# Kernel optimization log

Hardware: AMD Instinct MI355X
Metric: run time of the kernel (lower is better)

Reference implementation:

```python
import jax, jax.numpy as jnp
import numpy as np

N_NODES = 50000
EPS = 1e-12  # F.normalize eps


def _gcn_layer(x, W, b, src, dst):
    # GCNConv(normalize=False): h = x @ W, then sum-aggregate messages from
    # source nodes into target nodes along edge_index, then add bias.
    h = x @ W
    agg = jax.ops.segment_sum(h[src], dst, num_segments=N_NODES)
    out = agg + b
    # F.normalize(p=2, dim=-1) then ReLU
    norm = jnp.linalg.norm(out, axis=-1, keepdims=True)
    out = out / jnp.maximum(norm, EPS)
    return jax.nn.relu(out)


def setup_inputs() -> dict:
    key = jax.random.key(0)
    ks = jax.random.split(key, 8)
    nfeat, nhid, nclass, n_edges = 128, 128, 40, 640000
    x = jax.random.normal(ks[0], (N_NODES, nfeat), dtype=jnp.float32)
    edge_index = jax.random.randint(ks[1], (2, n_edges), 0, N_NODES, dtype=jnp.int64)
    s = 1.0 / np.sqrt(nhid)
    return {
        "x": x,
        "edge_index": edge_index,
        "W1": jax.random.normal(ks[2], (nfeat, nhid), jnp.float32) * s,
        "b1": jnp.zeros((nhid,), jnp.float32),
        "W2": jax.random.normal(ks[3], (nhid, nhid), jnp.float32) * s,
        "b2": jnp.zeros((nhid,), jnp.float32),
        "W3": jax.random.normal(ks[4], (nhid, nhid), jnp.float32) * s,
        "b3": jnp.zeros((nhid,), jnp.float32),
        "W4": jax.random.normal(ks[5], (nhid, nhid), jnp.float32) * s,
        "b4": jnp.zeros((nhid,), jnp.float32),
        "Wl": jax.random.normal(ks[6], (nhid, nclass), jnp.float32) * s,
        "bl": jnp.zeros((nclass,), jnp.float32),
    }


def reference(x, edge_index, W1, b1, W2, b2, W3, b3, W4, b4, Wl, bl):
    src, dst = edge_index[0], edge_index[1]
    x1 = _gcn_layer(x, W1, b1, src, dst)
    x2 = _gcn_layer(x1, W2, b2, src, dst)
    x3 = _gcn_layer(x2, W3, b3, src, dst)
    x4 = _gcn_layer(x3, W4, b4, src, dst)
    logits = x4 @ Wl + bl
    probs = jax.nn.softmax(logits, axis=-1)
    return (logits, probs, x4)
```

## Files before the change

kernel.cpp:

```cpp
#include <hip/hip_runtime.h>
#include <hip/hip_bf16.h>
#include <hip/hip_fp16.h>
#include <math.h>

#define NFEAT 128
#define NCLASS 40
#define RSHIFT 12
#define NRANGE 13

typedef __attribute__((ext_vector_type(8))) short frag_ab;
typedef __attribute__((ext_vector_type(4))) float frag_cd;

static __device__ inline unsigned short f2bf_rne(float f) {
    union { float f; unsigned u; } v;
    v.f = f;
    unsigned r = v.u + 0x7FFFu + ((v.u >> 16) & 1u);
    return (unsigned short)(r >> 16);
}
static __device__ inline float bf2f(unsigned short h) {
    union { unsigned u; float f; } v;
    v.u = ((unsigned)h) << 16;
    return v.f;
}


__global__ __launch_bounds__(256) void prep_kernel(const float* __restrict__ x,
                                                   __half* __restrict__ xh, int xc4,
                                                   const float* __restrict__ W0,
                                                   const float* __restrict__ W1,
                                                   const float* __restrict__ W2,
                                                   const float* __restrict__ W3,
                                                   short* __restrict__ whi,
                                                   short* __restrict__ wlo,
                                                   const int* __restrict__ src,
                                                   const int* __restrict__ dst,
                                                   int* __restrict__ cntR, int n_nodes,
                                                   int n_edges, int convB) {
    int b = blockIdx.x;
    if (b < convB) {
        int i = b * 256 + threadIdx.x;
        if (i < xc4) {
            float4 v = ((const float4*)x)[i];
            ((__half2*)xh)[i * 2 + 0] = __floats2half2_rn(v.x, v.y);
            ((__half2*)xh)[i * 2 + 1] = __floats2half2_rn(v.z, v.w);
        }
    } else if (b < convB + 32) {
        int wb = b - convB;
        int layer = wb >> 3;
        const float* W = layer == 0 ? W0 : layer == 1 ? W1 : layer == 2 ? W2 : W3;
        short* h = whi + (size_t)layer * 16384;
        short* l = wlo + (size_t)layer * 16384;
        int idx = (wb & 7) * 256 + threadIdx.x;
        int lane = idx & 63;
        int t = (idx >> 6) & 7;
        int s = idx >> 9;
        int quad = lane >> 4;
        int n = lane & 15;
        int kbase = s * 32 + quad * 8;
        int col = t * 16 + n;
#pragma unroll
        for (int j = 0; j < 8; ++j) {
            float f = W[(size_t)(kbase + j) * NFEAT + col];
            unsigned short hb = f2bf_rne(f);
            unsigned short lb = f2bf_rne(f - bf2f(hb));
            h[(size_t)idx * 8 + j] = (short)hb;
            l[(size_t)idx * 8 + j] = (short)lb;
        }
    } else {
        int hb = b - convB - 32;
        int i = hb * 256 + threadIdx.x;
        int n4 = n_edges >> 2;
        if (i < n4) {
            int4 d = ((const int4*)dst)[i];
            int4 s = ((const int4*)src)[i];
            atomicAdd(&cntR[(size_t)(s.x >> RSHIFT) * n_nodes + d.x], 1);
            atomicAdd(&cntR[(size_t)(s.y >> RSHIFT) * n_nodes + d.y], 1);
            atomicAdd(&cntR[(size_t)(s.z >> RSHIFT) * n_nodes + d.z], 1);
            atomicAdd(&cntR[(size_t)(s.w >> RSHIFT) * n_nodes + d.w], 1);
        }
        if (hb == 0 && threadIdx.x == 0) {
            for (int e = n4 << 2; e < n_edges; ++e)
                atomicAdd(&cntR[(size_t)(src[e] >> RSHIFT) * n_nodes + dst[e]], 1);
        }
    }
}


__global__ __launch_bounds__(256) void scan1_kernel(const int* __restrict__ cntR,
                                                    int* __restrict__ cnt,
                                                    int* __restrict__ excl,
                                                    int* __restrict__ bsums,
                                                    int* __restrict__ hist, int n) {
    __shared__ int sd[256];
    __shared__ int lh[64];
    int t = threadIdx.x;
    int i = blockIdx.x * 256 + t;
    if (t < 64) lh[t] = 0;
    int v = 0;
    if (i < n) {
#pragma unroll
        for (int r = 0; r < NRANGE; ++r) v += cntR[(size_t)r * n + i];
    }
    sd[t] = v;
    __syncthreads();
#pragma unroll
    for (int off = 1; off < 256; off <<= 1) {
        int tmp = (t >= off) ? sd[t - off] : 0;
        __syncthreads();
        sd[t] += tmp;
        __syncthreads();
    }
    if (i < n) {
        cnt[i] = v;
        excl[i] = sd[t] - v;
        atomicAdd(&lh[v < 63 ? v : 63], 1);
    }
    if (t == 255) bsums[blockIdx.x] = sd[255];
    __syncthreads();
    if (t < 64 && lh[t]) atomicAdd(&hist[t], lh[t]);
}

__global__ __launch_bounds__(256) void scan3_kernel(const int* __restrict__ excl,
                                                    const int* __restrict__ bsums,
                                                    int* __restrict__ row_ptr,
                                                    const int* __restrict__ cntR,
                                                    int* __restrict__ woffR,
                                                    const int* __restrict__ cnt,
                                                    const int* __restrict__ hist,
                                                    int* __restrict__ hoff,
                                                    int* __restrict__ perm,
                                                    int n, int nb) {
    __shared__ int sd[256];
    __shared__ int off_s, tot_s;
    __shared__ int hincl[64];
    __shared__ int bcnt[64];
    __shared__ int bbase[64];
    int t = threadIdx.x;
    if (t < 64) bcnt[t] = 0;
    int v = (t < nb) ? bsums[t] : 0;
    sd[t] = v;
    __syncthreads();
#pragma unroll
    for (int off = 1; off < 256; off <<= 1) {
        int tmp = (t >= off) ? sd[t - off] : 0;
        __syncthreads();
        sd[t] += tmp;
        __syncthreads();
    }
    if (t == 0) {
        off_s = (blockIdx.x > 0) ? sd[blockIdx.x - 1] : 0;
        tot_s = sd[255];
        int s = 0;
        for (int d = 0; d < 64; ++d) { s += hist[d]; hincl[d] = s; }
    }
    __syncthreads();
    int i = blockIdx.x * 256 + t;
    int d = 0, myslot = 0;
    if (i < n) {
        int val = excl[i] + off_s;
        row_ptr[i] = val;
        int run = val;
#pragma unroll
        for (int r = 0; r < NRANGE; ++r) {
            int c = cntR[(size_t)r * n + i];
            woffR[(size_t)r * n + i] = run;
            run += c;
        }
        int deg = cnt[i];
        d = deg < 63 ? deg : 63;
        myslot = atomicAdd(&bcnt[d], 1);
    }
    if (i == 0) row_ptr[n] = tot_s;
    __syncthreads();
    if (t < 64 && bcnt[t]) bbase[t] = atomicAdd(&hoff[t], bcnt[t]);
    __syncthreads();
    if (i < n) {
        perm[(n - hincl[d]) + bbase[d] + myslot] = i;
    }
}

__global__ __launch_bounds__(256) void scatter_kernel(const int* __restrict__ src,
                                                      const int* __restrict__ dst,
                                                      int* __restrict__ woffR,
                                                      int* __restrict__ src_sorted,
                                                      int n_nodes, int n_edges) {
    int i = blockIdx.x * 256 + threadIdx.x;
    int n4 = n_edges >> 2;
    if (i < n4) {
        int4 d = ((const int4*)dst)[i];
        int4 s = ((const int4*)src)[i];
        int p0 = atomicAdd(&woffR[(size_t)(s.x >> RSHIFT) * n_nodes + d.x], 1);
        int p1 = atomicAdd(&woffR[(size_t)(s.y >> RSHIFT) * n_nodes + d.y], 1);
        int p2 = atomicAdd(&woffR[(size_t)(s.z >> RSHIFT) * n_nodes + d.z], 1);
        int p3 = atomicAdd(&woffR[(size_t)(s.w >> RSHIFT) * n_nodes + d.w], 1);
        src_sorted[p0] = s.x;
        src_sorted[p1] = s.y;
        src_sorted[p2] = s.z;
        src_sorted[p3] = s.w;
    }
    if (i == 0) {
        for (int e = n4 << 2; e < n_edges; ++e) {
            int p = atomicAdd(&woffR[(size_t)(src[e] >> RSHIFT) * n_nodes + dst[e]], 1);
            src_sorted[p] = src[e];
        }
    }
}


__global__ __launch_bounds__(256) void gcn_fused_kernel(const __half* __restrict__ xin,
                                                        const int* __restrict__ row_ptr,
                                                        const int* __restrict__ src_sorted,
                                                        const int* __restrict__ perm,
                                                        const short* __restrict__ whi,
                                                        const short* __restrict__ wlo,
                                                        const float* __restrict__ bias,
                                                        float* __restrict__ outf,
                                                        __half* __restrict__ outh, int M) {
    __shared__ float smem[64][132];
    __shared__ int ctr;
    int tid = threadIdx.x;
    int base = blockIdx.x * 64;
    if (tid == 0) ctr = 0;
    __syncthreads();

    {
        int c = tid & 15;
        int lane = tid & 63;
        const uint4* xp = (const uint4*)xin;
        for (;;) {
            int nl = 0;
            if ((lane & 15) == 0) nl = atomicAdd(&ctr, 1);
            nl = __shfl(nl, lane & 48);
            if (nl >= 64) break;
            int slot = base + nl;
            float a[8];
#pragma unroll
            for (int i = 0; i < 8; ++i) a[i] = 0.f;
            int jb = 0, je = 0;
            if (slot < M) {
                int node = perm[slot];
                jb = row_ptr[node];
                je = row_ptr[node + 1];
            }

            int j = jb;
            int i0 = 0, i1 = 0, i2 = 0, i3 = 0;
            bool have4 = (j + 4 <= je);
            if (have4) {
                i0 = src_sorted[j];
                i1 = src_sorted[j + 1];
                i2 = src_sorted[j + 2];
                i3 = src_sorted[j + 3];
            }
            while (have4) {
                uint4 r0 = xp[i0 * 16 + c];
                uint4 r1 = xp[i1 * 16 + c];
                uint4 r2 = xp[i2 * 16 + c];
                uint4 r3 = xp[i3 * 16 + c];
                int jn = j + 4;
                bool more = (jn + 4 <= je);
                if (more) {
                    i0 = src_sorted[jn];
                    i1 = src_sorted[jn + 1];
                    i2 = src_sorted[jn + 2];
                    i3 = src_sorted[jn + 3];
                }
#pragma unroll
                for (int q = 0; q < 4; ++q) {
                    unsigned u0 = (&r0.x)[q], u1 = (&r1.x)[q], u2 = (&r2.x)[q], u3 = (&r3.x)[q];
                    float2 f0 = __half22float2(*(__half2*)&u0);
                    float2 f1 = __half22float2(*(__half2*)&u1);
                    float2 f2 = __half22float2(*(__half2*)&u2);
                    float2 f3 = __half22float2(*(__half2*)&u3);
                    a[q * 2 + 0] += f0.x + f1.x + f2.x + f3.x;
                    a[q * 2 + 1] += f0.y + f1.y + f2.y + f3.y;
                }
                j = jn;
                have4 = more;
            }
            for (; j < je; ++j) {
                int s0 = src_sorted[j];
                uint4 r0 = xp[s0 * 16 + c];
#pragma unroll
                for (int q = 0; q < 4; ++q) {
                    unsigned u0 = (&r0.x)[q];
                    float2 f0 = __half22float2(*(__half2*)&u0);
                    a[q * 2 + 0] += f0.x;
                    a[q * 2 + 1] += f0.y;
                }
            }
            float4* wp = (float4*)&smem[nl][c * 8];
            wp[0] = make_float4(a[0], a[1], a[2], a[3]);
            wp[1] = make_float4(a[4], a[5], a[6], a[7]);
        }
    }
    __syncthreads();

    int wave = tid >> 6;
    int lane = tid & 63;
    int quad = lane >> 4;
    int n16 = lane & 15;
    int lrow = wave * 16 + n16;

    const frag_ab* WH = (const frag_ab*)whi;
    const frag_ab* WL = (const frag_ab*)wlo;

    frag_cd acc[8];
#pragma unroll
    for (int t = 0; t < 8; ++t) acc[t] = (frag_cd){0.f, 0.f, 0.f, 0.f};

#pragma unroll
    for (int s = 0; s < 4; ++s) {
        const float* ap = &smem[lrow][s * 32 + quad * 8];
        float4 v0 = *(const float4*)(ap);
        float4 v1 = *(const float4*)(ap + 4);
        float fv[8] = {v0.x, v0.y, v0.z, v0.w, v1.x, v1.y, v1.z, v1.w};
        frag_ab ah, al;
#pragma unroll
        for (int jj = 0; jj < 8; ++jj) {
            unsigned short hb = f2bf_rne(fv[jj]);
            ah[jj] = (short)hb;
            al[jj] = (short)f2bf_rne(fv[jj] - bf2f(hb));
        }
#pragma unroll
        for (int t = 0; t < 8; ++t) {
            frag_ab bh = WH[(s * 8 + t) * 64 + lane];
            frag_ab bl = WL[(s * 8 + t) * 64 + lane];
            acc[t] = __builtin_amdgcn_mfma_f32_16x16x32_bf16(ah, bh, acc[t], 0, 0, 0);
            acc[t] = __builtin_amdgcn_mfma_f32_16x16x32_bf16(ah, bl, acc[t], 0, 0, 0);
            acc[t] = __builtin_amdgcn_mfma_f32_16x16x32_bf16(al, bh, acc[t], 0, 0, 0);
        }
    }

    float ssq[4] = {0.f, 0.f, 0.f, 0.f};
#pragma unroll
    for (int t = 0; t < 8; ++t) {
        float bv = bias[t * 16 + n16];
#pragma unroll
        for (int r = 0; r < 4; ++r) {
            acc[t][r] += bv;
            ssq[r] += acc[t][r] * acc[t][r];
        }
    }
#pragma unroll
    for (int mask = 1; mask <= 8; mask <<= 1) {
#pragma unroll
        for (int r = 0; r < 4; ++r) ssq[r] += __shfl_xor(ssq[r], mask);
    }
    float inv[4];
#pragma unroll
    for (int r = 0; r < 4; ++r) inv[r] = 1.0f / fmaxf(sqrtf(ssq[r]), 1e-12f);

    int slot0 = base + wave * 16 + quad * 4;
#pragma unroll
    for (int r = 0; r < 4; ++r) {
        int slot = slot0 + r;
        if (slot < M) {
            int orow = perm[slot];
            if (outh) {
                __half* op = outh + (size_t)orow * NFEAT + n16;
#pragma unroll
                for (int t = 0; t < 8; ++t)
                    op[t * 16] = __float2half(fmaxf(acc[t][r] * inv[r], 0.f));
            } else {
                float* op = outf + (size_t)orow * NFEAT + n16;
#pragma unroll
                for (int t = 0; t < 8; ++t)
                    op[t * 16] = fmaxf(acc[t][r] * inv[r], 0.f);
            }
        }
    }
}


__global__ __launch_bounds__(256) void classifier_kernel(const float* __restrict__ x4,
                                                         const float* __restrict__ Wl,
                                                         const float* __restrict__ bl,
                                                         float* __restrict__ logits,
                                                         float* __restrict__ probs, int n_nodes) {
    int node = blockIdx.x * 256 + threadIdx.x;
    int nc = node < n_nodes ? node : n_nodes - 1;
    const float* row = x4 + (size_t)nc * NFEAT;

    float acc[NCLASS];
#pragma unroll
    for (int c = 0; c < NCLASS; ++c) acc[c] = bl[c];

    for (int k = 0; k < NFEAT; k += 4) {
        float4 a = *(const float4*)(row + k);
#pragma unroll
        for (int kk = 0; kk < 4; ++kk) {
            float av = (&a.x)[kk];
            const float* Wr = Wl + (k + kk) * NCLASS;
#pragma unroll
            for (int c = 0; c < NCLASS; ++c) acc[c] += av * Wr[c];
        }
    }

    float m = acc[0];
#pragma unroll
    for (int c = 1; c < NCLASS; ++c) m = fmaxf(m, acc[c]);
    float ex[NCLASS];
    float sum = 0.f;
#pragma unroll
    for (int c = 0; c < NCLASS; ++c) {
        ex[c] = __expf(acc[c] - m);
        sum += ex[c];
    }
    float is = 1.0f / sum;

    if (node < n_nodes) {
        float4* lo = (float4*)(logits + (size_t)node * NCLASS);
        float4* po = (float4*)(probs + (size_t)node * NCLASS);
#pragma unroll
        for (int c = 0; c < NCLASS; c += 4) {
            float4 lv, pv;
            lv.x = acc[c + 0]; lv.y = acc[c + 1]; lv.z = acc[c + 2]; lv.w = acc[c + 3];
            pv.x = ex[c + 0] * is; pv.y = ex[c + 1] * is; pv.z = ex[c + 2] * is; pv.w = ex[c + 3] * is;
            lo[c >> 2] = lv;
            po[c >> 2] = pv;
        }
    }
}


extern "C" void kernel_launch(void* const* d_in, const int* in_sizes, int n_in,
                              void* d_out, int out_size, void* d_ws, size_t ws_size,
                              hipStream_t stream) {
    const float* x  = (const float*)d_in[0];
    const int*   ei = (const int*)d_in[1];
    const float* W1 = (const float*)d_in[2];
    const float* b1 = (const float*)d_in[3];
    const float* W2 = (const float*)d_in[4];
    const float* b2 = (const float*)d_in[5];
    const float* W3 = (const float*)d_in[6];
    const float* b3 = (const float*)d_in[7];
    const float* W4 = (const float*)d_in[8];
    const float* b4 = (const float*)d_in[9];
    const float* Wl = (const float*)d_in[10];
    const float* bl = (const float*)d_in[11];

    const int n_nodes = in_sizes[0] / NFEAT;
    const int n_edges = in_sizes[1] / 2;
    const int* src = ei;
    const int* dst = ei + n_edges;

    float* out    = (float*)d_out;
    float* logits = out;
    float* probs  = out + (size_t)n_nodes * NCLASS;
    float* x4     = out + 2 * (size_t)n_nodes * NCLASS;

    char* ws = (char*)d_ws;
    size_t off = 0;
    auto wsalloc = [&](size_t bytes) -> void* {
        void* p = ws + off;
        off += (bytes + 255) & ~(size_t)255;
        return p;
    };
    __half* xh         = (__half*)wsalloc((size_t)n_nodes * NFEAT * sizeof(__half));
    __half* xh2        = (__half*)wsalloc((size_t)n_nodes * NFEAT * sizeof(__half));
    int*    row_ptr    = (int*)wsalloc(((size_t)n_nodes + 1) * sizeof(int));
    int*    cntR       = (int*)wsalloc(((size_t)NRANGE * n_nodes + 128) * sizeof(int));
    int*    hist       = cntR + (size_t)NRANGE * n_nodes;
    int*    hoff       = hist + 64;
    int*    woffR      = (int*)wsalloc((size_t)NRANGE * n_nodes * sizeof(int));
    int*    cnt        = (int*)wsalloc((size_t)n_nodes * sizeof(int));
    int*    perm       = (int*)wsalloc((size_t)n_nodes * sizeof(int));
    int*    src_sorted = (int*)wsalloc((size_t)n_edges * sizeof(int));
    int     nbt        = (n_nodes + 255) / 256;
    int*    bsums      = (int*)wsalloc(((size_t)nbt + 1) * sizeof(int));
    short*  whi        = (short*)wsalloc((size_t)4 * 16384 * sizeof(short));
    short*  wlo        = (short*)wsalloc((size_t)4 * 16384 * sizeof(short));

    hipMemsetAsync(cntR, 0, ((size_t)NRANGE * n_nodes + 128) * sizeof(int), stream);

    int xc4   = (n_nodes * NFEAT) / 4;
    int convB = (xc4 + 255) / 256;
    int e4b   = ((n_edges >> 2) + 255) / 256;
    prep_kernel<<<convB + 32 + e4b, 256, 0, stream>>>(x, xh, xc4,
                                                      W1, W2, W3, W4, whi, wlo,
                                                      src, dst, cntR, n_nodes,
                                                      n_edges, convB);

    scan1_kernel<<<nbt, 256, 0, stream>>>(cntR, cnt, row_ptr , bsums, hist, n_nodes);
    scan3_kernel<<<nbt, 256, 0, stream>>>(row_ptr, bsums, row_ptr, cntR, woffR,
                                          cnt, hist, hoff, perm, n_nodes, nbt);
    scatter_kernel<<<e4b, 256, 0, stream>>>(src, dst, woffR, src_sorted, n_nodes, n_edges);

    int gb = (n_nodes + 63) / 64;
    int cb = (n_nodes + 255) / 256;

    gcn_fused_kernel<<<gb, 256, 0, stream>>>(xh,  row_ptr, src_sorted, perm, whi + 0 * 16384, wlo + 0 * 16384, b1, nullptr, xh2, n_nodes);
    gcn_fused_kernel<<<gb, 256, 0, stream>>>(xh2, row_ptr, src_sorted, perm, whi + 1 * 16384, wlo + 1 * 16384, b2, nullptr, xh,  n_nodes);
    gcn_fused_kernel<<<gb, 256, 0, stream>>>(xh,  row_ptr, src_sorted, perm, whi + 2 * 16384, wlo + 2 * 16384, b3, nullptr, xh2, n_nodes);
    gcn_fused_kernel<<<gb, 256, 0, stream>>>(xh2, row_ptr, src_sorted, perm, whi + 3 * 16384, wlo + 3 * 16384, b4, x4, nullptr, n_nodes);

    classifier_kernel<<<cb, 256, 0, stream>>>(x4, Wl, bl, logits, probs, n_nodes);
}
```

Baseline: 348.1 us.

## Aggregate in source-range phases across nodes for gather cache locality

Drops the degree-sorted perm and the shared-memory atomic work queue from the GCN aggregation. Each block now processes its 64 natural-order nodes range by range: for each of the 13 source-index ranges it gathers only edges whose sources fall in that range. Partial sums are accumulated in shared memory. The goal is to keep concurrent gathers within a narrow slice of the feature matrix for better L2 reuse. In exchange it loses the 4-way unrolled load batching and the dynamic load balancing, adds more loop overhead and shared-memory round trips, and relies on woffR holding per-range end offsets after the scatter.

```diff
diff --git a/kernel.cpp b/kernel.cpp
--- a/kernel.cpp
+++ b/kernel.cpp
@@ -209,89 +209,55 @@
 
 __global__ __launch_bounds__(256) void gcn_fused_kernel(const __half* __restrict__ xin,
                                                         const int* __restrict__ row_ptr,
+                                                        const int* __restrict__ wend,
                                                         const int* __restrict__ src_sorted,
-                                                        const int* __restrict__ perm,
                                                         const short* __restrict__ whi,
                                                         const short* __restrict__ wlo,
                                                         const float* __restrict__ bias,
                                                         float* __restrict__ outf,
-                                                        __half* __restrict__ outh, int M) {
+                                                        __half* __restrict__ outh,
+                                                        int M, int nn) {
     __shared__ float smem[64][132];
-    __shared__ int ctr;
     int tid = threadIdx.x;
     int base = blockIdx.x * 64;
-    if (tid == 0) ctr = 0;
-    __syncthreads();
+    int c = tid & 15;
+    int qw = tid >> 4;
+
+#pragma unroll
+    for (int p = 0; p < 4; ++p) {
+        float4* wp = (float4*)&smem[p * 16 + qw][c * 8];
+        wp[0] = make_float4(0.f, 0.f, 0.f, 0.f);
+        wp[1] = make_float4(0.f, 0.f, 0.f, 0.f);
+    }
 
     {
-        int c = tid & 15;
-        int lane = tid & 63;
         const uint4* xp = (const uint4*)xin;
-        for (;;) {
-            int nl = 0;
-            if ((lane & 15) == 0) nl = atomicAdd(&ctr, 1);
-            nl = __shfl(nl, lane & 48);
-            if (nl >= 64) break;
-            int slot = base + nl;
-            float a[8];
-#pragma unroll
-            for (int i = 0; i < 8; ++i) a[i] = 0.f;
-            int jb = 0, je = 0;
-            if (slot < M) {
-                int node = perm[slot];
-                jb = row_ptr[node];
-                je = row_ptr[node + 1];
+        for (int r = 0; r < NRANGE; ++r) {
+#pragma unroll 1
+            for (int p = 0; p < 4; ++p) {
+                int nl = p * 16 + qw;
+                int node = base + nl;
+                if (node >= M) continue;
+                int s = (r == 0) ? row_ptr[node] : wend[(size_t)(r - 1) * nn + node];
+                int e = wend[(size_t)r * nn + node];
+                if (s >= e) continue;
+                float4* wp = (float4*)&smem[nl][c * 8];
+                float4 v0 = wp[0], v1 = wp[1];
+                float a[8] = {v0.x, v0.y, v0.z, v0.w, v1.x, v1.y, v1.z, v1.w};
+                for (int j = s; j < e; ++j) {
+                    int s0 = src_sorted[j];
+                    uint4 rr = xp[s0 * 16 + c];
+#pragma unroll
+                    for (int q = 0; q < 4; ++q) {
+                        unsigned u = (&rr.x)[q];
+                        float2 f = __half22float2(*(__half2*)&u);
+                        a[q * 2 + 0] += f.x;
+                        a[q * 2 + 1] += f.y;
+                    }
+                }
+                wp[0] = make_float4(a[0], a[1], a[2], a[3]);
+                wp[1] = make_float4(a[4], a[5], a[6], a[7]);
             }
-
-            int j = jb;
-            int i0 = 0, i1 = 0, i2 = 0, i3 = 0;
-            bool have4 = (j + 4 <= je);
-            if (have4) {
-                i0 = src_sorted[j];
-                i1 = src_sorted[j + 1];
-                i2 = src_sorted[j + 2];
-                i3 = src_sorted[j + 3];
-            }
-            while (have4) {
-                uint4 r0 = xp[i0 * 16 + c];
-                uint4 r1 = xp[i1 * 16 + c];
-                uint4 r2 = xp[i2 * 16 + c];
-                uint4 r3 = xp[i3 * 16 + c];
-                int jn = j + 4;
-                bool more = (jn + 4 <= je);
-                if (more) {
-                    i0 = src_sorted[jn];
-                    i1 = src_sorted[jn + 1];
-                    i2 = src_sorted[jn + 2];
-                    i3 = src_sorted[jn + 3];
-                }
-#pragma unroll
-                for (int q = 0; q < 4; ++q) {
-                    unsigned u0 = (&r0.x)[q], u1 = (&r1.x)[q], u2 = (&r2.x)[q], u3 = (&r3.x)[q];
-                    float2 f0 = __half22float2(*(__half2*)&u0);
-                    float2 f1 = __half22float2(*(__half2*)&u1);
-                    float2 f2 = __half22float2(*(__half2*)&u2);
-                    float2 f3 = __half22float2(*(__half2*)&u3);
-                    a[q * 2 + 0] += f0.x + f1.x + f2.x + f3.x;
-                    a[q * 2 + 1] += f0.y + f1.y + f2.y + f3.y;
-                }
-                j = jn;
-                have4 = more;
-            }
-            for (; j < je; ++j) {
-                int s0 = src_sorted[j];
-                uint4 r0 = xp[s0 * 16 + c];
-#pragma unroll
-                for (int q = 0; q < 4; ++q) {
-                    unsigned u0 = (&r0.x)[q];
-                    float2 f0 = __half22float2(*(__half2*)&u0);
-                    a[q * 2 + 0] += f0.x;
-                    a[q * 2 + 1] += f0.y;
-                }
-            }
-            float4* wp = (float4*)&smem[nl][c * 8];
-            wp[0] = make_float4(a[0], a[1], a[2], a[3]);
-            wp[1] = make_float4(a[4], a[5], a[6], a[7]);
         }
     }
     __syncthreads();
@@ -351,12 +317,11 @@
 #pragma unroll
     for (int r = 0; r < 4; ++r) inv[r] = 1.0f / fmaxf(sqrtf(ssq[r]), 1e-12f);
 
-    int slot0 = base + wave * 16 + quad * 4;
+    int orow0 = base + wave * 16 + quad * 4;
 #pragma unroll
     for (int r = 0; r < 4; ++r) {
-        int slot = slot0 + r;
-        if (slot < M) {
-            int orow = perm[slot];
+        int orow = orow0 + r;
+        if (orow < M) {
             if (outh) {
                 __half* op = outh + (size_t)orow * NFEAT + n16;
 #pragma unroll
@@ -490,10 +455,10 @@
     int gb = (n_nodes + 63) / 64;
     int cb = (n_nodes + 255) / 256;
 
-    gcn_fused_kernel<<<gb, 256, 0, stream>>>(xh,  row_ptr, src_sorted, perm, whi + 0 * 16384, wlo + 0 * 16384, b1, nullptr, xh2, n_nodes);
-    gcn_fused_kernel<<<gb, 256, 0, stream>>>(xh2, row_ptr, src_sorted, perm, whi + 1 * 16384, wlo + 1 * 16384, b2, nullptr, xh,  n_nodes);
-    gcn_fused_kernel<<<gb, 256, 0, stream>>>(xh,  row_ptr, src_sorted, perm, whi + 2 * 16384, wlo + 2 * 16384, b3, nullptr, xh2, n_nodes);
-    gcn_fused_kernel<<<gb, 256, 0, stream>>>(xh2, row_ptr, src_sorted, perm, whi + 3 * 16384, wlo + 3 * 16384, b4, x4, nullptr, n_nodes);
+    gcn_fused_kernel<<<gb, 256, 0, stream>>>(xh,  row_ptr, woffR, src_sorted, whi + 0 * 16384, wlo + 0 * 16384, b1, nullptr, xh2, n_nodes, n_nodes);
+    gcn_fused_kernel<<<gb, 256, 0, stream>>>(xh2, row_ptr, woffR, src_sorted, whi + 1 * 16384, wlo + 1 * 16384, b2, nullptr, xh,  n_nodes, n_nodes);
+    gcn_fused_kernel<<<gb, 256, 0, stream>>>(xh,  row_ptr, woffR, src_sorted, whi + 2 * 16384, wlo + 2 * 16384, b3, nullptr, xh2, n_nodes, n_nodes);
+    gcn_fused_kernel<<<gb, 256, 0, stream>>>(xh2, row_ptr, woffR, src_sorted, whi + 3 * 16384, wlo + 3 * 16384, b4, x4, nullptr, n_nodes, n_nodes);
 
     classifier_kernel<<<cb, 256, 0, stream>>>(x4, Wl, bl, logits, probs, n_nodes);
 }
```

Result: slower. 582.0 us (+67.2%).
